# Kernel optimization log

Measured on AMD Instinct MI355X. Metric: run time of the kernel, lower is better.

The kernel has to match this reference:

```python
import jax, jax.numpy as jnp
import numpy as np

NH = 12
D = 768
HD = D // NH
F = 3072
EPS = 1e-6
SCALE = 1.0 / np.sqrt(HD).astype(np.float32)


def _ln(x, g, b):
    m = x.mean(-1, keepdims=True)
    v = ((x - m) ** 2).mean(-1, keepdims=True)
    return (x - m) / jnp.sqrt(v + EPS) * g + b


def _heads(t):
    B, S, _ = t.shape
    return t.reshape(B, S, NH, HD).transpose(0, 2, 1, 3)  # [B,H,S,hd]


def _attn(q, k, v):
    # q,k,v: [B,H,S,hd]; dropout rate is 0 so omitted
    s = jnp.einsum('bhqd,bhkd->bhqk', q, k) * SCALE
    p = jax.nn.softmax(s, axis=-1)
    c = jnp.einsum('bhqk,bhkd->bhqd', p, v)
    B, H, S, _ = c.shape
    return c.transpose(0, 2, 1, 3).reshape(B, S, D)


def _mlp(x, W1, b1, W2, b2):
    h = jax.nn.gelu(x @ W1 + b1)  # dropout rate 0.1 -> identity (eval)
    return h @ W2 + b2


def setup_inputs() -> dict:
    key = jax.random.key(0)
    ks = jax.random.split(key, 16)
    B, S = 4, 1024
    rnd = lambda k, sh: (jax.random.normal(k, sh, jnp.float32) * 0.02)
    inp = {
        'x': jax.random.normal(ks[0], (B, S, D), jnp.float32),
        'y': jax.random.normal(ks[1], (B, S, D), jnp.float32),
        'ln1x_g': jnp.ones((D,)), 'ln1x_b': jnp.zeros((D,)),
        'ln1y_g': jnp.ones((D,)), 'ln1y_b': jnp.zeros((D,)),
        'Wq': rnd(ks[2], (D, D)), 'bq': jnp.zeros((D,)),
        'Wk': rnd(ks[3], (D, D)), 'bk': jnp.zeros((D,)),
        'Wv': rnd(ks[4], (D, D)), 'bv': jnp.zeros((D,)),
        'Wo': rnd(ks[5], (D, D)), 'bo': jnp.zeros((D,)),
        'Wqd': rnd(ks[6], (D, D)), 'bqd': jnp.zeros((D,)),
        'Wkd': rnd(ks[7], (D, D)), 'bkd': jnp.zeros((D,)),
        'Wvd': rnd(ks[8], (D, D)), 'bvd': jnp.zeros((D,)),
        'Wod': rnd(ks[9], (D, D)), 'bod': jnp.zeros((D,)),
        'w11': jnp.full((1,), 0.5), 'w12': jnp.full((1,), 0.5),
        'w21': jnp.full((1,), 0.5), 'w22': jnp.full((1,), 0.5),
        'ln2x_g': jnp.ones((D,)), 'ln2x_b': jnp.zeros((D,)),
        'ln2y_g': jnp.ones((D,)), 'ln2y_b': jnp.zeros((D,)),
        'W1': rnd(ks[10], (D, F)), 'b1': jnp.zeros((F,)),
        'W2': rnd(ks[11], (F, D)), 'b2': jnp.zeros((D,)),
        'W1d': rnd(ks[12], (D, F)), 'b1d': jnp.zeros((F,)),
        'W2d': rnd(ks[13], (F, D)), 'b2d': jnp.zeros((D,)),
    }
    return inp


def reference(x, y, ln1x_g, ln1x_b, ln1y_g, ln1y_b,
              Wq, bq, Wk, bk, Wv, bv, Wo, bo,
              Wqd, bqd, Wkd, bkd, Wvd, bvd, Wod, bod,
              w11, w12, w21, w22,
              ln2x_g, ln2x_b, ln2y_g, ln2y_b,
              W1, b1, W2, b2, W1d, b1d, W2d, b2d):
    hx, hy = x, y
    xn = _ln(x, ln1x_g, ln1x_b)
    yn = _ln(y, ln1y_g, ln1y_b)
    q = _heads(xn @ Wq + bq); k = _heads(xn @ Wk + bk); v = _heads(xn @ Wv + bv)
    qd = _heads(yn @ Wqd + bqd); kd = _heads(yn @ Wkd + bkd); vd = _heads(yn @ Wvd + bvd)
    a_sx = _attn(q, k, v) @ Wo + bo          # self-x
    a_sy = _attn(qd, kd, vd) @ Wod + bod     # self-y
    a_cx = _attn(q, kd, vd) @ Wo + bo        # cross x-query into y
    a_cy = _attn(qd, k, v) @ Wod + bod       # cross y-query into x
    ax = w11 * a_sx + w12 * a_cx
    ay = w21 * a_sy + w22 * a_cy
    x = ax + hx
    y = ay + hy
    hx, hy = x, y
    x = _mlp(_ln(x, ln2x_g, ln2x_b), W1, b1, W2, b2) + hx
    y = _mlp(_ln(y, ln2y_g, ln2y_b), W1d, b1d, W2d, b2d) + hy
    return (x, y)
```

## Files before the change

kernel.cpp:

```cpp
#include <hip/hip_runtime.h>

typedef unsigned short u16;
typedef unsigned short u16x8 __attribute__((ext_vector_type(8)));
typedef short s16x8 __attribute__((ext_vector_type(8)));
typedef float f32x4 __attribute__((ext_vector_type(4)));

#define EL ((size_t)3145728)
#define DDE ((size_t)589824)
#define DFE ((size_t)2359296)

#if __has_builtin(__builtin_amdgcn_exp2f)
#define EXP2(x) __builtin_amdgcn_exp2f(x)
#else
#define EXP2(x) __expf((x) * 0.6931471805599453f)
#endif

__device__ __forceinline__ float b2f(u16 u) {
    return __builtin_bit_cast(float, (unsigned)u << 16);
}
__device__ __forceinline__ u16 f2bf(float f) {
    unsigned x = __builtin_bit_cast(unsigned, f);
    return (u16)((x + 0x7fffu + ((x >> 16) & 1u)) >> 16);
}
__device__ __forceinline__ float gelu_f(float x) {
    float t = x + 0.044715f * x * x * x;
    return x * __builtin_amdgcn_rcpf(1.0f + EXP2(-2.302207417f * t));
}
__device__ __forceinline__ f32x4 mfma16(s16x8 a, s16x8 b, f32x4 c) {
    return __builtin_amdgcn_mfma_f32_16x16x32_bf16(a, b, c, 0, 0, 0);
}
__device__ __forceinline__ void gld16(const u16* g, u16* l) {
    __builtin_amdgcn_global_load_lds((const __attribute__((address_space(1))) void*)g,
                                     (__attribute__((address_space(3))) void*)l,
                                     16, 0, 0);
}
__device__ __forceinline__ void xcd_map(int NN, int& m, int& n, int& z, int& ks) {
    int p = blockIdx.x, T = gridDim.x;
    int ppx = T >> 3;
    int xcd = p & 7, l = p >> 3;
    int panel = l / NN;
    n = l - panel * NN;
    int gp = xcd * (ppx / NN) + panel;
    m = gp & 31;
    z = (gp >> 5) & 1;
    ks = gp >> 6;
}

__global__ __launch_bounds__(256) void transpose8_k(const float* p0, const float* p1,
                                                    const float* p2, const float* p3,
                                                    const float* p4, const float* p5,
                                                    const float* p6, const float* p7,
                                                    u16* __restrict__ dst0) {
    int z = blockIdx.z;
    const float* in = z == 0 ? p0 : z == 1 ? p1 : z == 2 ? p2 : z == 3 ? p3
                    : z == 4 ? p4 : z == 5 ? p5 : z == 6 ? p6 : p7;
    u16* out = dst0 + (size_t)z * DDE;
    const int K = 768, N = 768;
    __shared__ u16 tile[64][72];
    int k0 = blockIdx.y << 6, n0 = blockIdx.x << 6;
    int tid = threadIdx.x;
    int r = tid >> 2, c = (tid & 3) << 4;
    const float* ip = in + (size_t)(k0 + r) * N + n0 + c;
#pragma unroll
    for (int q = 0; q < 4; ++q) {
        f32x4 v = *(const f32x4*)(ip + 4 * q);
#pragma unroll
        for (int e = 0; e < 4; ++e) tile[r][c + 4 * q + e] = f2bf(v[e]);
    }
    __syncthreads();
    u16x8 o0, o1;
#pragma unroll
    for (int e = 0; e < 8; ++e) { o0[e] = tile[c + e][r]; o1[e] = tile[c + 8 + e][r]; }
    u16* op = out + (size_t)(n0 + r) * K + k0 + c;
    *(u16x8*)op = o0;
    *(u16x8*)(op + 8) = o1;
}

__global__ __launch_bounds__(256) void transpose2_k(const float* pa, const float* pb,
                                                    u16* __restrict__ dst0, size_t dsz,
                                                    int K, int N) {
    int z = blockIdx.z;
    const float* in = z ? pb : pa;
    u16* out = dst0 + (size_t)z * dsz;
    __shared__ u16 tile[64][72];
    int k0 = blockIdx.y << 6, n0 = blockIdx.x << 6;
    int tid = threadIdx.x;
    int r = tid >> 2, c = (tid & 3) << 4;
    const float* ip = in + (size_t)(k0 + r) * N + n0 + c;
#pragma unroll
    for (int q = 0; q < 4; ++q) {
        f32x4 v = *(const f32x4*)(ip + 4 * q);
#pragma unroll
        for (int e = 0; e < 4; ++e) tile[r][c + 4 * q + e] = f2bf(v[e]);
    }
    __syncthreads();
    u16x8 o0, o1;
#pragma unroll
    for (int e = 0; e < 8; ++e) { o0[e] = tile[c + e][r]; o1[e] = tile[c + 8 + e][r]; }
    u16* op = out + (size_t)(n0 + r) * K + k0 + c;
    *(u16x8*)op = o0;
    *(u16x8*)(op + 8) = o1;
}

__global__ __launch_bounds__(256) void ln_k(const float* __restrict__ inX,
                                            const float* __restrict__ inY,
                                            const float* gX, const float* bX,
                                            const float* gY, const float* bY,
                                            u16* __restrict__ out0) {
    int z = blockIdx.y;
    const float* in = z ? inY : inX;
    const float* g = z ? gY : gX;
    const float* be = z ? bY : bX;
    u16* out = out0 + (size_t)z * EL;
    int row = blockIdx.x, tid = threadIdx.x;
    const float* p = in + (size_t)row * 768;
    float v0 = p[tid], v1 = p[tid + 256], v2 = p[tid + 512];
    float s = v0 + v1 + v2;
    float q = v0 * v0 + v1 * v1 + v2 * v2;
#pragma unroll
    for (int m = 1; m < 64; m <<= 1) { s += __shfl_xor(s, m); q += __shfl_xor(q, m); }
    __shared__ float red[8];
    int w = tid >> 6, lane = tid & 63;
    if (lane == 0) { red[w] = s; red[4 + w] = q; }
    __syncthreads();
    s = red[0] + red[1] + red[2] + red[3];
    q = red[4] + red[5] + red[6] + red[7];
    float mean = s * (1.0f / 768.0f);
    float var = q * (1.0f / 768.0f) - mean * mean;
    float rstd = rsqrtf(var + 1e-6f);
    u16* o = out + (size_t)row * 768;
    o[tid]       = f2bf((v0 - mean) * rstd * g[tid]       + be[tid]);
    o[tid + 256] = f2bf((v1 - mean) * rstd * g[tid + 256] + be[tid + 256]);
    o[tid + 512] = f2bf((v2 - mean) * rstd * g[tid + 512] + be[tid + 512]);
}

__global__ __launch_bounds__(256) void lnb_init_k(const u16* __restrict__ inX,
                                                  const u16* __restrict__ inY,
                                                  const float* gX, const float* bX,
                                                  const float* gY, const float* bY,
                                                  const float* b2X, const float* b2Y,
                                                  u16* __restrict__ out0,
                                                  float* __restrict__ outF0) {
    int z = blockIdx.y;
    const u16* in = z ? inY : inX;
    const float* g = z ? gY : gX;
    const float* be = z ? bY : bX;
    const float* bb = z ? b2Y : b2X;
    u16* out = out0 + (size_t)z * EL;
    float* of = outF0 + (size_t)z * EL;
    int row = blockIdx.x, tid = threadIdx.x;
    const u16* p = in + (size_t)row * 768;
    float v0 = b2f(p[tid]), v1 = b2f(p[tid + 256]), v2 = b2f(p[tid + 512]);
    float s = v0 + v1 + v2;
    float q = v0 * v0 + v1 * v1 + v2 * v2;
#pragma unroll
    for (int m = 1; m < 64; m <<= 1) { s += __shfl_xor(s, m); q += __shfl_xor(q, m); }
    __shared__ float red[8];
    int w = tid >> 6, lane = tid & 63;
    if (lane == 0) { red[w] = s; red[4 + w] = q; }
    __syncthreads();
    s = red[0] + red[1] + red[2] + red[3];
    q = red[4] + red[5] + red[6] + red[7];
    float mean = s * (1.0f / 768.0f);
    float var = q * (1.0f / 768.0f) - mean * mean;
    float rstd = rsqrtf(var + 1e-6f);
    u16* o = out + (size_t)row * 768;
    float* f = of + (size_t)row * 768;
    o[tid]       = f2bf((v0 - mean) * rstd * g[tid]       + be[tid]);
    o[tid + 256] = f2bf((v1 - mean) * rstd * g[tid + 256] + be[tid + 256]);
    o[tid + 512] = f2bf((v2 - mean) * rstd * g[tid + 512] + be[tid + 512]);
    f[tid]       = v0 + bb[tid];
    f[tid + 256] = v1 + bb[tid + 256];
    f[tid + 512] = v2 + bb[tid + 512];
}

__global__ __launch_bounds__(256) void blend_k(u16* __restrict__ a0,
                                               const u16* __restrict__ b0,
                                               const float* w11, const float* w12,
                                               const float* w21, const float* w22,
                                               int n8) {
    int z = blockIdx.z;
    u16* a = a0 + (size_t)z * EL;
    const u16* b = b0 + (size_t)z * EL;
    float wa = z ? *w21 : *w11, wb = z ? *w22 : *w12;
    for (int i = blockIdx.x * blockDim.x + threadIdx.x; i < n8;
         i += gridDim.x * blockDim.x) {
        u16x8 va = ((const u16x8*)a)[i];
        u16x8 vb = ((const u16x8*)b)[i];
        u16x8 r;
#pragma unroll
        for (int e = 0; e < 8; ++e) r[e] = f2bf(wa * b2f(va[e]) + wb * b2f(vb[e]));
        ((u16x8*)a)[i] = r;
    }
}

#define EPI_GELU 3
#define EPI_WO 4
#define EPI_SK 5

template <int EPI>
__global__ __launch_bounds__(256) void gemm_k(
    const u16* __restrict__ A0, size_t Asz,
    const u16* __restrict__ B0, size_t Bsz,
    const float* __restrict__ bias0, const float* __restrict__ bias1,
    const void* __restrict__ r0, const void* __restrict__ r1,
    const float* s1a, const float* s1b, const float* s2a, const float* s2b,
    void* __restrict__ C0, size_t Csz,
    int M, int N, int K, int NN, int KS) {
    int m_, n_, z, ks;
    xcd_map(NN, m_, n_, z, ks);
    const int Kloc = K / KS;
    const u16* A = A0 + z * Asz;
    const u16* BT = B0 + z * Bsz;
    const float* bias = z ? bias1 : bias0;
    const float* residf = (const float*)(z ? r1 : r0);
    u16* Cb = (u16*)C0 + z * Csz;
    float* Cf = (float*)C0 + z * Csz;
    __shared__ u16 lA[2][4096];
    __shared__ u16 lB[2][4096];
    int tid = threadIdx.x;
    int bm0 = m_ << 7, bn0 = n_ << 7;
    int lane = tid & 63, wid = tid >> 6;
    int fr = lane & 15, g = lane >> 4;
    int wm = wid >> 1, wn = wid & 1;
    const u16* srcA0 = A + (size_t)(bm0 + (tid & 127)) * K + ks * Kloc + ((tid >> 7) << 3);
    const u16* srcA1 = srcA0 + 16;
    const u16* srcB0 = BT + (size_t)(bn0 + (tid & 127)) * K + ks * Kloc + ((tid >> 7) << 3);
    const u16* srcB1 = srcB0 + 16;
    auto STAGE = [&](int buf, int k0) {
        gld16(srcA0 + k0, &lA[buf][0] + tid * 8);
        gld16(srcA1 + k0, &lA[buf][0] + 2048 + tid * 8);
        gld16(srcB0 + k0, &lB[buf][0] + tid * 8);
        gld16(srcB1 + k0, &lB[buf][0] + 2048 + tid * 8);
    };
    f32x4 acc[4][4] = {};
    STAGE(0, 0);
    __syncthreads();
    int cur = 0;
    for (int k0 = 0; k0 < Kloc; k0 += 32) {
        if (k0 + 32 < Kloc) STAGE(cur ^ 1, k0 + 32);
        s16x8 af[4], bf[4];
#pragma unroll
        for (int i = 0; i < 4; ++i)
            af[i] = *(const s16x8*)&lA[cur][(g * 128 + wm * 64 + i * 16 + fr) * 8];
#pragma unroll
        for (int j = 0; j < 4; ++j)
            bf[j] = *(const s16x8*)&lB[cur][(g * 128 + wn * 64 + j * 16 + fr) * 8];
#pragma unroll
        for (int i = 0; i < 4; ++i)
#pragma unroll
            for (int j = 0; j < 4; ++j)
                acc[i][j] = mfma16(af[i], bf[j], acc[i][j]);
        __syncthreads();
        cur ^= 1;
    }
    float bscale = 1.0f;
    if (EPI == EPI_WO) bscale = z ? (s2a[0] + s2b[0]) : (s1a[0] + s1b[0]);
#pragma unroll
    for (int j = 0; j < 4; ++j) {
        int n = bn0 + wn * 64 + j * 16 + fr;
        float bv = 0.0f;
        if (EPI != EPI_SK) bv = bias[n] * bscale;
#pragma unroll
        for (int i = 0; i < 4; ++i) {
#pragma unroll
            for (int r = 0; r < 4; ++r) {
                int m = bm0 + wm * 64 + i * 16 + (g << 2) + r;
                size_t idx = (size_t)m * N + n;
                float v = acc[i][j][r] + bv;
                if (EPI == EPI_GELU) {
                    Cb[idx] = f2bf(gelu_f(v));
                } else if (EPI == EPI_WO) {
                    Cb[idx] = f2bf(v + residf[idx]);
                } else {
                    unsafeAtomicAdd(&Cf[idx], v);
                }
            }
        }
    }
}

__global__ __launch_bounds__(256) void gemm_qkv_k(const u16* __restrict__ A0,
                                                  const u16* __restrict__ B0,
                                                  const float* bq, const float* bk,
                                                  const float* bv, const float* bqd,
                                                  const float* bkd, const float* bvd,
                                                  u16* __restrict__ Qd,
                                                  u16* __restrict__ Kd,
                                                  u16* __restrict__ Vd) {
    const int K = 768;
    int m_, n_, z, ks_;
    xcd_map(18, m_, n_, z, ks_);
    const u16* A = A0 + z * EL;
    const u16* BT = B0 + z * 3 * DDE;
    __shared__ u16 lA[2][4096];
    __shared__ u16 lB[2][4096];
    int tid = threadIdx.x;
    int bm0 = m_ << 7, bn0 = n_ << 7;
    int lane = tid & 63, wid = tid >> 6, wm = wid >> 1, wn = wid & 1;
    int fr = lane & 15, g = lane >> 4;
    const u16* srcA0 = A + (size_t)(bm0 + (tid & 127)) * K + ((tid >> 7) << 3);
    const u16* srcA1 = srcA0 + 16;
    const u16* srcB0 = BT + (size_t)(bn0 + (tid & 127)) * K + ((tid >> 7) << 3);
    const u16* srcB1 = srcB0 + 16;
    auto STAGE = [&](int buf, int k0) {
        gld16(srcA0 + k0, &lA[buf][0] + tid * 8);
        gld16(srcA1 + k0, &lA[buf][0] + 2048 + tid * 8);
        gld16(srcB0 + k0, &lB[buf][0] + tid * 8);
        gld16(srcB1 + k0, &lB[buf][0] + 2048 + tid * 8);
    };
    f32x4 acc[4][4] = {};
    STAGE(0, 0);
    __syncthreads();
    int cur = 0;
    for (int k0 = 0; k0 < K; k0 += 32) {
        if (k0 + 32 < K) STAGE(cur ^ 1, k0 + 32);
        s16x8 af[4], bf[4];
#pragma unroll
        for (int i = 0; i < 4; ++i)
            af[i] = *(const s16x8*)&lA[cur][(g * 128 + wm * 64 + i * 16 + fr) * 8];
#pragma unroll
        for (int j = 0; j < 4; ++j)
            bf[j] = *(const s16x8*)&lB[cur][(g * 128 + wn * 64 + j * 16 + fr) * 8];
#pragma unroll
        for (int i = 0; i < 4; ++i)
#pragma unroll
            for (int j = 0; j < 4; ++j)
                acc[i][j] = mfma16(af[i], bf[j], acc[i][j]);
        __syncthreads();
        cur ^= 1;
    }
    int seg = bn0 / 768;
    const float* bp = seg == 0 ? (z ? bqd : bq) : seg == 1 ? (z ? bkd : bk) : (z ? bvd : bv);
    u16* out = (seg == 0 ? Qd : seg == 1 ? Kd : Vd) + (size_t)z * 3 * EL;
    int nbase = bn0 - seg * 768;
    const float qs = 0.180336880f;
#pragma unroll
    for (int j = 0; j < 4; ++j) {
        int nn = nbase + wn * 64 + j * 16 + fr;
        float bvl = bp[nn];
        int hh = nn >> 6, hd = nn & 63;
#pragma unroll
        for (int i = 0; i < 4; ++i) {
#pragma unroll
            for (int r = 0; r < 4; ++r) {
                int m = bm0 + wm * 64 + i * 16 + (g << 2) + r;
                int bb = m >> 10, ss = m & 1023;
                size_t o = ((size_t)(bb * 12 + hh)) << 16;
                if (seg < 2) o += ((size_t)ss << 6) + hd;
                else         o += ((size_t)hd << 10) + ss;
                float v = acc[i][j][r] + bvl;
                if (seg == 0) v *= qs;
                out[o] = f2bf(v);
            }
        }
    }
}

__global__ __launch_bounds__(256) void attn_k(const u16* __restrict__ Qx,
                                              const u16* __restrict__ Kx,
                                              const u16* __restrict__ VTx,
                                              const u16* __restrict__ Qy,
                                              const u16* __restrict__ Ky,
                                              const u16* __restrict__ VTy,
                                              u16* __restrict__ csx,
                                              u16* __restrict__ ccx,
                                              u16* __restrict__ csy,
                                              u16* __restrict__ ccy) {
    int p = blockIdx.x;
    int lg = (p & 7) * 192 + (p >> 3);
    int sg = lg >> 4, wi = lg & 15;
    int qt = wi & 7, sub = wi >> 3;
    int pairi = sg / 48, bh = sg % 48;
    int cfg = pairi == 0 ? (sub ? 3 : 0) : (sub ? 2 : 1);
    const u16 *Qp, *Kp, *Vp;
    u16* Op;
    if (cfg == 0)      { Qp = Qx; Kp = Kx; Vp = VTx; Op = csx; }
    else if (cfg == 1) { Qp = Qy; Kp = Ky; Vp = VTy; Op = csy; }
    else if (cfg == 2) { Qp = Qx; Kp = Ky; Vp = VTy; Op = ccx; }
    else               { Qp = Qy; Kp = Kx; Vp = VTx; Op = ccy; }
    const u16* Qh = Qp + ((size_t)bh << 16);
    const u16* Kh = Kp + ((size_t)bh << 16);
    const u16* Vh = Vp + ((size_t)bh << 16);
    int b = bh / 12, h = bh % 12;
    int tid = threadIdx.x, lane = tid & 63, w = tid >> 6;
    int q0 = qt * 128 + w * 32;
    int fr = lane & 15, ko = (lane >> 4) << 3, g = lane >> 4;
    bool glo = lane < 32;
    int srcA = fr + ((lane & 16) << 1);
    int srcB = srcA + 16;

    __shared__ u16 kls[2048];
    __shared__ u16 vls[2048];

    s16x8 qf[2][2];
#pragma unroll
    for (int s = 0; s < 2; ++s) {
        const u16* qp = Qh + (size_t)(q0 + s * 16 + fr) * 64 + ko;
        qf[s][0] = *(const s16x8*)qp;
        qf[s][1] = *(const s16x8*)(qp + 32);
    }

    f32x4 acc[2][4] = {};
    float lsum[2] = {0.f, 0.f};
    f32x4 zz = {0.f, 0.f, 0.f, 0.f};

    int krow = tid >> 3, kpc = tid & 7;
    int kgc = kpc ^ (krow & 7);
    int vdr = tid >> 2, vpv = tid & 3;
    int cK0 = ((fr << 3) + (g ^ (fr & 7))) << 3;
    int cK1 = ((fr << 3) + ((g + 4) ^ (fr & 7))) << 3;
    int cK2 = (((fr + 16) << 3) + (g ^ (fr & 7))) << 3;
    int cK3 = (((fr + 16) << 3) + ((g + 4) ^ (fr & 7))) << 3;

    for (int kb = 0; kb < 1024; kb += 32) {
        gld16(Kh + (size_t)(kb + krow) * 64 + kgc * 8, &kls[tid * 8]);
        gld16(Vh + (size_t)vdr * 1024 + kb + vpv * 8, &vls[tid * 8]);
        __syncthreads();
        s16x8 Kf0 = *(const s16x8*)&kls[cK0];
        s16x8 Kf1 = *(const s16x8*)&kls[cK1];
        s16x8 Kf2 = *(const s16x8*)&kls[cK2];
        s16x8 Kf3 = *(const s16x8*)&kls[cK3];
        s16x8 Vf[4];
#pragma unroll
        for (int t4 = 0; t4 < 4; ++t4)
            Vf[t4] = *(const s16x8*)&vls[((t4 * 16 + fr) << 5) + (g << 3)];
        s16x8 pa[2];
#pragma unroll
        for (int s = 0; s < 2; ++s) {
            __builtin_amdgcn_s_setprio(1);
            f32x4 t0 = mfma16(Kf0, qf[s][0], zz);
            t0 = mfma16(Kf1, qf[s][1], t0);
            f32x4 t1 = mfma16(Kf2, qf[s][0], zz);
            t1 = mfma16(Kf3, qf[s][1], t1);
            __builtin_amdgcn_s_setprio(0);
            float p00 = EXP2(t0[0]), p01 = EXP2(t0[1]);
            float p02 = EXP2(t0[2]), p03 = EXP2(t0[3]);
            float p10 = EXP2(t1[0]), p11 = EXP2(t1[1]);
            float p12 = EXP2(t1[2]), p13 = EXP2(t1[3]);
            lsum[s] += (p00 + p01 + p02 + p03) + (p10 + p11 + p12 + p13);
            unsigned w0, w1, w2, w3;
            asm("v_cvt_pk_bf16_f32 %0, %1, %2" : "=v"(w0) : "v"(p00), "v"(p01));
            asm("v_cvt_pk_bf16_f32 %0, %1, %2" : "=v"(w1) : "v"(p02), "v"(p03));
            asm("v_cvt_pk_bf16_f32 %0, %1, %2" : "=v"(w2) : "v"(p10), "v"(p11));
            asm("v_cvt_pk_bf16_f32 %0, %1, %2" : "=v"(w3) : "v"(p12), "v"(p13));
            int e0 = __shfl((int)w0, srcA), e1 = __shfl((int)w1, srcA);
            int e2 = __shfl((int)w0, srcB), e3 = __shfl((int)w1, srcB);
            int f0 = __shfl((int)w2, srcA), f1 = __shfl((int)w3, srcA);
            int f2 = __shfl((int)w2, srcB), f3 = __shfl((int)w3, srcB);
            int4 wd;
            wd.x = glo ? e0 : f0;
            wd.y = glo ? e1 : f1;
            wd.z = glo ? e2 : f2;
            wd.w = glo ? e3 : f3;
            pa[s] = __builtin_bit_cast(s16x8, wd);
        }
        __builtin_amdgcn_s_setprio(1);
#pragma unroll
        for (int t4 = 0; t4 < 4; ++t4) {
            acc[0][t4] = mfma16(pa[0], Vf[t4], acc[0][t4]);
            acc[1][t4] = mfma16(pa[1], Vf[t4], acc[1][t4]);
        }
        __builtin_amdgcn_s_setprio(0);
        __syncthreads();
    }

    float invv[2][4];
#pragma unroll
    for (int s = 0; s < 2; ++s) {
        float l = lsum[s];
        l += __shfl_xor(l, 16);
        l += __shfl_xor(l, 32);
        float inv = 1.0f / l;
#pragma unroll
        for (int r = 0; r < 4; ++r)
            invv[s][r] = __shfl(inv, ((lane >> 4) << 2) + r);
    }
#pragma unroll
    for (int s = 0; s < 2; ++s) {
        u16* ob = Op + (size_t)(b * 1024 + q0 + s * 16 + ((lane >> 4) << 2)) * 768 + h * 64 + fr;
#pragma unroll
        for (int t4 = 0; t4 < 4; ++t4)
#pragma unroll
            for (int r = 0; r < 4; ++r)
                ob[(size_t)r * 768 + t4 * 16] = f2bf(acc[s][t4][r] * invv[s][r]);
    }
}

extern "C" void kernel_launch(void* const* d_in, const int* in_sizes, int n_in,
                              void* d_out, int out_size, void* d_ws, size_t ws_size,
                              hipStream_t stream) {
    (void)in_sizes; (void)n_in; (void)out_size; (void)ws_size;
    const float* X    = (const float*)d_in[0];
    const float* Y    = (const float*)d_in[1];
    const float* l1xg = (const float*)d_in[2];
    const float* l1xb = (const float*)d_in[3];
    const float* l1yg = (const float*)d_in[4];
    const float* l1yb = (const float*)d_in[5];
    const float* Wq   = (const float*)d_in[6];
    const float* bq   = (const float*)d_in[7];
    const float* Wk   = (const float*)d_in[8];
    const float* bk   = (const float*)d_in[9];
    const float* Wv   = (const float*)d_in[10];
    const float* bv   = (const float*)d_in[11];
    const float* Wo   = (const float*)d_in[12];
    const float* bo   = (const float*)d_in[13];
    const float* Wqd  = (const float*)d_in[14];
    const float* bqd  = (const float*)d_in[15];
    const float* Wkd  = (const float*)d_in[16];
    const float* bkd  = (const float*)d_in[17];
    const float* Wvd  = (const float*)d_in[18];
    const float* bvd  = (const float*)d_in[19];
    const float* Wod  = (const float*)d_in[20];
    const float* bod  = (const float*)d_in[21];
    const float* w11  = (const float*)d_in[22];
    const float* w12  = (const float*)d_in[23];
    const float* w21  = (const float*)d_in[24];
    const float* w22  = (const float*)d_in[25];
    const float* l2xg = (const float*)d_in[26];
    const float* l2xb = (const float*)d_in[27];
    const float* l2yg = (const float*)d_in[28];
    const float* l2yb = (const float*)d_in[29];
    const float* W1   = (const float*)d_in[30];
    const float* b1   = (const float*)d_in[31];
    const float* W2   = (const float*)d_in[32];
    const float* b2   = (const float*)d_in[33];
    const float* W1d  = (const float*)d_in[34];
    const float* b1d  = (const float*)d_in[35];
    const float* W2d  = (const float*)d_in[36];
    const float* b2d  = (const float*)d_in[37];

    u16* ws = (u16*)d_ws;
    u16* qkvT = ws;
    u16* WoT  = qkvT + 6 * DDE;
    u16* W1T  = WoT + 2 * DDE;
    u16* W2T  = W1T + 2 * DFE;
    u16* xn   = W2T + 2 * DFE;
    u16* Qx   = xn + 2 * EL;
    u16* cs   = Qx + 6 * EL;
    u16* x1   = cs + 4 * EL;
    u16* Kx = Qx + EL;
    u16* VTx = Qx + 2 * EL;
    u16* Qy = Qx + 3 * EL;
    u16* Ky = Qx + 4 * EL;
    u16* VTy = Qx + 5 * EL;
    u16* h = Qx;
    u16* y1 = x1 + EL;

    float* out_x = (float*)d_out;

    dim3 tb(256);
    transpose8_k<<<dim3(12, 12, 8), tb, 0, stream>>>(Wq, Wk, Wv, Wqd, Wkd, Wvd, Wo, Wod, qkvT);
    transpose2_k<<<dim3(48, 12, 2), tb, 0, stream>>>(W1, W1d, W1T, DFE, 768, 3072);
    transpose2_k<<<dim3(12, 48, 2), tb, 0, stream>>>(W2, W2d, W2T, DFE, 3072, 768);
    ln_k<<<dim3(4096, 2), tb, 0, stream>>>(X, Y, l1xg, l1xb, l1yg, l1yb, xn);
    gemm_qkv_k<<<1152, tb, 0, stream>>>(xn, qkvT, bq, bk, bv, bqd, bkd, bvd,
                                        Qx, Kx, VTx);
    attn_k<<<4 * 48 * 8, tb, 0, stream>>>(Qx, Kx, VTx, Qy, Ky, VTy,
                                          cs, cs + 2 * EL, cs + EL, cs + 3 * EL);
    int n8 = (int)(EL / 8);
    blend_k<<<dim3(1536, 1, 2), tb, 0, stream>>>(cs, cs + 2 * EL, w11, w12, w21, w22, n8);
    gemm_k<EPI_WO><<<384, tb, 0, stream>>>(
        cs, EL, WoT, DDE, bo, bod, X, Y, w11, w12, w21, w22, x1, EL,
        4096, 768, 768, 6, 1);
    lnb_init_k<<<dim3(4096, 2), tb, 0, stream>>>(x1, y1, l2xg, l2xb, l2yg, l2yb,
                                                 b2, b2d, xn, out_x);
    gemm_k<EPI_GELU><<<1536, tb, 0, stream>>>(
        xn, EL, W1T, DFE, b1, b1d, nullptr, nullptr, nullptr, nullptr, nullptr, nullptr,
        h, 4 * EL, 4096, 3072, 768, 24, 1);
    gemm_k<EPI_SK><<<1536, tb, 0, stream>>>(
        h, 4 * EL, W2T, DFE, nullptr, nullptr, nullptr, nullptr,
        nullptr, nullptr, nullptr, nullptr,
        out_x, EL, 4096, 768, 3072, 6, 4);
}
```

Before: 462.4 us.

## Replace atomic split-K accumulation with partial buffers and combine kernel

The final MLP down-projection GEMM no longer uses float atomics into the output initialized by the LayerNorm kernel. Each K-split now writes plain stores into its own partial buffer in workspace, and a new combine kernel sums the partials and adds bias and residual. If workspace is too small, it falls back to a single-pass GEMM whose epilogue adds bias and residual directly. This removes atomic contention and the output pre-initialization, at the cost of extra partial-buffer traffic and one more launch.

```diff
diff --git a/kernel.cpp b/kernel.cpp
--- a/kernel.cpp
+++ b/kernel.cpp
@@ -134,20 +134,16 @@
     o[tid + 512] = f2bf((v2 - mean) * rstd * g[tid + 512] + be[tid + 512]);
 }
 
-__global__ __launch_bounds__(256) void lnb_init_k(const u16* __restrict__ inX,
-                                                  const u16* __restrict__ inY,
-                                                  const float* gX, const float* bX,
-                                                  const float* gY, const float* bY,
-                                                  const float* b2X, const float* b2Y,
-                                                  u16* __restrict__ out0,
-                                                  float* __restrict__ outF0) {
+__global__ __launch_bounds__(256) void lnb_k(const u16* __restrict__ inX,
+                                             const u16* __restrict__ inY,
+                                             const float* gX, const float* bX,
+                                             const float* gY, const float* bY,
+                                             u16* __restrict__ out0) {
     int z = blockIdx.y;
     const u16* in = z ? inY : inX;
     const float* g = z ? gY : gX;
     const float* be = z ? bY : bX;
-    const float* bb = z ? b2Y : b2X;
     u16* out = out0 + (size_t)z * EL;
-    float* of = outF0 + (size_t)z * EL;
     int row = blockIdx.x, tid = threadIdx.x;
     const u16* p = in + (size_t)row * 768;
     float v0 = b2f(p[tid]), v1 = b2f(p[tid + 256]), v2 = b2f(p[tid + 512]);
@@ -165,13 +161,9 @@
     float var = q * (1.0f / 768.0f) - mean * mean;
     float rstd = rsqrtf(var + 1e-6f);
     u16* o = out + (size_t)row * 768;
-    float* f = of + (size_t)row * 768;
     o[tid]       = f2bf((v0 - mean) * rstd * g[tid]       + be[tid]);
     o[tid + 256] = f2bf((v1 - mean) * rstd * g[tid + 256] + be[tid + 256]);
     o[tid + 512] = f2bf((v2 - mean) * rstd * g[tid + 512] + be[tid + 512]);
-    f[tid]       = v0 + bb[tid];
-    f[tid + 256] = v1 + bb[tid + 256];
-    f[tid + 512] = v2 + bb[tid + 512];
 }
 
 __global__ __launch_bounds__(256) void blend_k(u16* __restrict__ a0,
@@ -194,9 +186,33 @@
     }
 }
 
+__global__ __launch_bounds__(256) void combine_k(const float* __restrict__ parts,
+                                                 int KS,
+                                                 const u16* __restrict__ x1b,
+                                                 const float* __restrict__ b2X,
+                                                 const float* __restrict__ b2Y,
+                                                 float* __restrict__ out, int n4tot) {
+    int i = blockIdx.x * 256 + threadIdx.x;
+    if (i >= n4tot) return;
+    size_t e = (size_t)i * 4;
+    f32x4 s = ((const f32x4*)parts)[i];
+    for (int k = 1; k < KS; ++k)
+        s += ((const f32x4*)(parts + (size_t)k * 2 * EL))[i];
+    const float* bb = (e < EL) ? b2X : b2Y;
+    int n = (int)(e % 768);
+    ushort4 xv = ((const ushort4*)x1b)[i];
+    f32x4 r;
+    r[0] = s[0] + bb[n]     + b2f(xv.x);
+    r[1] = s[1] + bb[n + 1] + b2f(xv.y);
+    r[2] = s[2] + bb[n + 2] + b2f(xv.z);
+    r[3] = s[3] + bb[n + 3] + b2f(xv.w);
+    ((f32x4*)out)[i] = r;
+}
+
 #define EPI_GELU 3
 #define EPI_WO 4
-#define EPI_SK 5
+#define EPI_MLP2 5
+#define EPI_PART 6
 
 template <int EPI>
 __global__ __launch_bounds__(256) void gemm_k(
@@ -214,8 +230,9 @@
     const u16* BT = B0 + z * Bsz;
     const float* bias = z ? bias1 : bias0;
     const float* residf = (const float*)(z ? r1 : r0);
+    const u16* residb = (const u16*)(z ? r1 : r0);
     u16* Cb = (u16*)C0 + z * Csz;
-    float* Cf = (float*)C0 + z * Csz;
+    float* Cf = (float*)C0 + ((size_t)ks * 2 + z) * Csz;
     __shared__ u16 lA[2][4096];
     __shared__ u16 lB[2][4096];
     int tid = threadIdx.x;
@@ -260,7 +277,7 @@
     for (int j = 0; j < 4; ++j) {
         int n = bn0 + wn * 64 + j * 16 + fr;
         float bv = 0.0f;
-        if (EPI != EPI_SK) bv = bias[n] * bscale;
+        if (EPI != EPI_PART) bv = bias[n] * bscale;
 #pragma unroll
         for (int i = 0; i < 4; ++i) {
 #pragma unroll
@@ -272,8 +289,10 @@
                     Cb[idx] = f2bf(gelu_f(v));
                 } else if (EPI == EPI_WO) {
                     Cb[idx] = f2bf(v + residf[idx]);
+                } else if (EPI == EPI_MLP2) {
+                    Cf[idx] = v + b2f(residb[idx]);
                 } else {
-                    unsafeAtomicAdd(&Cf[idx], v);
+                    Cf[idx] = v;
                 }
             }
         }
@@ -490,7 +509,7 @@
 extern "C" void kernel_launch(void* const* d_in, const int* in_sizes, int n_in,
                               void* d_out, int out_size, void* d_ws, size_t ws_size,
                               hipStream_t stream) {
-    (void)in_sizes; (void)n_in; (void)out_size; (void)ws_size;
+    (void)in_sizes; (void)n_in; (void)out_size;
     const float* X    = (const float*)d_in[0];
     const float* Y    = (const float*)d_in[1];
     const float* l1xg = (const float*)d_in[2];
@@ -546,8 +565,16 @@
     u16* VTy = Qx + 5 * EL;
     u16* h = Qx;
     u16* y1 = x1 + EL;
+    u16* wsEnd = x1 + 2 * EL;
 
     float* out_x = (float*)d_out;
+
+    float* parts = (float*)wsEnd;
+    size_t baseBytes = (size_t)(wsEnd - ws) * 2;
+    size_t partBytes = 2 * EL * sizeof(float);
+    int KS = 1;
+    if (ws_size >= baseBytes + 4 * partBytes) KS = 4;
+    else if (ws_size >= baseBytes + 2 * partBytes) KS = 2;
 
     dim3 tb(256);
     transpose8_k<<<dim3(12, 12, 8), tb, 0, stream>>>(Wq, Wk, Wv, Wqd, Wkd, Wvd, Wo, Wod, qkvT);
@@ -563,13 +590,22 @@
     gemm_k<EPI_WO><<<384, tb, 0, stream>>>(
         cs, EL, WoT, DDE, bo, bod, X, Y, w11, w12, w21, w22, x1, EL,
         4096, 768, 768, 6, 1);
-    lnb_init_k<<<dim3(4096, 2), tb, 0, stream>>>(x1, y1, l2xg, l2xb, l2yg, l2yb,
-                                                 b2, b2d, xn, out_x);
+    lnb_k<<<dim3(4096, 2), tb, 0, stream>>>(x1, y1, l2xg, l2xb, l2yg, l2yb, xn);
     gemm_k<EPI_GELU><<<1536, tb, 0, stream>>>(
         xn, EL, W1T, DFE, b1, b1d, nullptr, nullptr, nullptr, nullptr, nullptr, nullptr,
         h, 4 * EL, 4096, 3072, 768, 24, 1);
-    gemm_k<EPI_SK><<<1536, tb, 0, stream>>>(
-        h, 4 * EL, W2T, DFE, nullptr, nullptr, nullptr, nullptr,
-        nullptr, nullptr, nullptr, nullptr,
-        out_x, EL, 4096, 768, 3072, 6, 4);
-}
+    if (KS > 1) {
+        gemm_k<EPI_PART><<<384 * KS, tb, 0, stream>>>(
+            h, 4 * EL, W2T, DFE, nullptr, nullptr, nullptr, nullptr,
+            nullptr, nullptr, nullptr, nullptr,
+            parts, EL, 4096, 768, 3072, 6, KS);
+        int n4 = (int)(2 * EL / 4);
+        combine_k<<<(n4 + 255) / 256, tb, 0, stream>>>(parts, KS, x1, b2, b2d,
+                                                       out_x, n4);
+    } else {
+        gemm_k<EPI_MLP2><<<384, tb, 0, stream>>>(
+            h, 4 * EL, W2T, DFE, b2, b2d, x1, y1,
+            nullptr, nullptr, nullptr, nullptr,
+            out_x, EL, 4096, 768, 3072, 6, 1);
+    }
+}
```

After: 448.8 us. -2.9%, faster.
